# Kernel optimization log

Measured on AMD Instinct MI355X. Metric: run time of the kernel, lower is better.

Reference implementation:

```python
import jax, jax.numpy as jnp
import numpy as np

B, N, D = 4, 2048, 512
H, DA, DL = 8, 64, 64  # heads, attention_dim, linear_dim
EPS = 1e-6


def _layer_norm(x, eps=EPS):
    # F.layer_norm with no affine params
    mu = jnp.mean(x, axis=-1, keepdims=True)
    var = jnp.var(x, axis=-1, keepdims=True)
    return (x - mu) * jax.lax.rsqrt(var + eps)


def setup_inputs() -> dict:
    key = jax.random.key(0)
    k1, k2, k3, k4 = jax.random.split(key, 4)
    x = jax.random.normal(k1, (B, N, D), dtype=jnp.float32)
    # causal (lower-triangular) valid-attention mask, float {0,1}, shape (B,1,N,N)
    attention_mask = jnp.broadcast_to(
        jnp.tril(jnp.ones((N, N), dtype=jnp.float32))[None, None], (B, 1, N, N)
    )
    # _uvqk: (D, 2*H*DL + 2*H*DA), init normal(0, 0.02)
    uvqk = 0.02 * jax.random.normal(k2, (D, 2 * H * DL + 2 * H * DA), dtype=jnp.float32)
    # _o: Linear(H*DL -> D), xavier uniform
    fan_in, fan_out = H * DL, D
    limit = float(np.sqrt(6.0 / (fan_in + fan_out)))
    o_weight = jax.random.uniform(k3, (fan_out, fan_in), dtype=jnp.float32, minval=-limit, maxval=limit)
    o_bias = jnp.zeros((D,), dtype=jnp.float32)
    return {"x": x, "attention_mask": attention_mask, "uvqk": uvqk,
            "o_weight": o_weight, "o_bias": o_bias}


def reference(x, attention_mask, uvqk, o_weight, o_bias):
    b, n, _ = x.shape
    normed_x = _layer_norm(x)
    mm = jax.nn.silu(normed_x @ uvqk)  # fused uvqk projection + silu
    u, v, q, k = jnp.split(mm, [H * DL, 2 * H * DL, 2 * H * DL + H * DA], axis=-1)
    qh = q.reshape(b, n, H, DA)
    kh = k.reshape(b, n, H, DA)
    vh = v.reshape(b, n, H, DL)
    # silu-activated (non-softmax) attention with mask
    qk = jnp.einsum('bnhd,bmhd->bhnm', qh, kh)
    qk = jax.nn.silu(qk) / n
    qk = qk * attention_mask  # (B,1,N,N) broadcast over heads
    attn = jnp.einsum('bhnm,bmhd->bnhd', qk, vh).reshape(b, n, H * DL)
    # gated norm + output proj + residual
    o_input = u * _layer_norm(attn)
    return o_input @ o_weight.T + o_bias + x
```

## Files before the change

### kernel.cpp

```cpp
#include <hip/hip_runtime.h>

typedef __bf16 bf16x8 __attribute__((ext_vector_type(8)));
typedef float f32x4 __attribute__((ext_vector_type(4)));
typedef float f32x16 __attribute__((ext_vector_type(16)));

__device__ __forceinline__ unsigned short f2bf(float f) {
  return __builtin_bit_cast(unsigned short, (__bf16)f);
}
__device__ __forceinline__ float bfu2f(unsigned short b) {
  unsigned int u = ((unsigned int)b) << 16;
  return __builtin_bit_cast(float, u);
}
__device__ __forceinline__ float silu_f(float x) {
  return x * __builtin_amdgcn_rcpf(1.0f + __expf(-x));
}
__device__ __forceinline__ unsigned pk2(float a, float b) {
  return (unsigned)f2bf(a) | ((unsigned)f2bf(b) << 16);
}

template<int CPR, int NI, int SWZ>
__device__ __forceinline__ void stage16(const __bf16* __restrict__ g, int ld,
                                        __bf16* lds, int wave, int lane) {
#pragma unroll
  for (int t = 0; t < NI; ++t) {
    int cb = (wave * NI + t) * 64;
    int c = cb + lane;
    int row = c / CPR;
    int colb = (c % CPR) ^ (row & SWZ);
    __builtin_amdgcn_global_load_lds(
        (const __attribute__((address_space(1))) unsigned int*)(g + row * ld + colb * 8),
        (__attribute__((address_space(3))) unsigned int*)(lds + cb * 8),
        16, 0, 0);
  }
}

__global__ void k_prep(const float* __restrict__ x, __bf16* __restrict__ nx,
                       const float* __restrict__ ow, __bf16* __restrict__ owb,
                       const float* __restrict__ uvqk, __bf16* __restrict__ uvqkT) {
  int bid = blockIdx.x, tid = threadIdx.x;
  if (bid < 4096) {
    int t = tid & 127;
    int r = bid * 2 + (tid >> 7);
    int wave = tid >> 6;
    float4 v = ((const float4*)(x + (size_t)r * 512))[t];
    float s = v.x + v.y + v.z + v.w;
    float ss = v.x * v.x + v.y * v.y + v.z * v.z + v.w * v.w;
#pragma unroll
    for (int o = 32; o > 0; o >>= 1) { s += __shfl_down(s, o); ss += __shfl_down(ss, o); }
    __shared__ float red[4][2];
    if ((tid & 63) == 0) { red[wave][0] = s; red[wave][1] = ss; }
    __syncthreads();
    int rw = (wave >> 1) * 2;
    s = red[rw][0] + red[rw + 1][0];
    ss = red[rw][1] + red[rw + 1][1];
    float mu = s * (1.0f / 512.0f);
    float var = ss * (1.0f / 512.0f) - mu * mu;
    float rs = rsqrtf(var + 1e-6f);
    ushort4 o4;
    o4.x = f2bf((v.x - mu) * rs); o4.y = f2bf((v.y - mu) * rs);
    o4.z = f2bf((v.z - mu) * rs); o4.w = f2bf((v.w - mu) * rs);
    ((ushort4*)(nx + (size_t)r * 512))[t] = o4;
  } else if (bid < 4352) {
    int i = (bid - 4096) * 256 + tid;
    float4 v = ((const float4*)ow)[i];
    ushort4 o4;
    o4.x = f2bf(v.x); o4.y = f2bf(v.y); o4.z = f2bf(v.z); o4.w = f2bf(v.w);
    ((ushort4*)owb)[i] = o4;
  } else {
    __shared__ float tile[32][33];
    int bb = bid - 4352;
    int n0 = (bb & 63) * 32, k0 = (bb >> 6) * 32;
    int tx = tid & 31, ty = tid >> 5;
    for (int i = ty; i < 32; i += 8)
      tile[i][tx] = uvqk[(k0 + i) * 2048 + n0 + tx];
    __syncthreads();
    for (int i = ty; i < 32; i += 8)
      uvqkT[(n0 + i) * 512 + k0 + tx] = (__bf16)tile[tx][i];
  }
}

__global__ __launch_bounds__(256, 2) void k_proj(
    const __bf16* __restrict__ A, const __bf16* __restrict__ Bt,
    __bf16* __restrict__ u, __bf16* __restrict__ qn,
    __bf16* __restrict__ kn, __bf16* __restrict__ vt) {
  __shared__ __bf16 As[128 * 64];
  __shared__ __bf16 Bs[256 * 64];
  int tid = threadIdx.x, wave = tid >> 6, lane = tid & 63;
  int lr = lane & 15, lq = lane >> 4;
  int bn = blockIdx.x, bm = blockIdx.y;
  const __bf16* Ag = A + (size_t)bm * 128 * 512;
  const __bf16* Bg = Bt + (size_t)bn * 256 * 512;
  int wm = (wave >> 1) * 64, wn2 = (wave & 1) * 128;
  f32x4 acc[4][8] = {};
  for (int k0 = 0; k0 < 512; k0 += 64) {
    stage16<8, 4, 7>(Ag + k0, 512, As, wave, lane);
    stage16<8, 8, 7>(Bg + k0, 512, Bs, wave, lane);
    __syncthreads();
#pragma unroll
    for (int kk = 0; kk < 2; ++kk) {
      int b = kk * 4 + lq;
      bf16x8 a[4], bb[8];
#pragma unroll
      for (int i = 0; i < 4; ++i) {
        int row = wm + i * 16 + lr;
        a[i] = *(const bf16x8*)(As + row * 64 + ((b ^ (row & 7)) * 8));
      }
#pragma unroll
      for (int j = 0; j < 8; ++j) {
        int row = wn2 + j * 16 + lr;
        bb[j] = *(const bf16x8*)(Bs + row * 64 + ((b ^ (row & 7)) * 8));
      }
#pragma unroll
      for (int i = 0; i < 4; ++i)
#pragma unroll
        for (int j = 0; j < 8; ++j)
          acc[i][j] = __builtin_amdgcn_mfma_f32_16x16x32_bf16(a[i], bb[j], acc[i][j], 0, 0, 0);
    }
    __syncthreads();
  }
  int seg = bn >> 1;
  int cb = (bn & 1) * 256 + wn2;
  int rb0 = bm * 128 + wm + lq * 4;
  if (seg == 1) {
#pragma unroll
    for (int i = 0; i < 4; ++i) {
      int rb = rb0 + i * 16;
      int b = rb >> 11, n = rb & 2047;
#pragma unroll
      for (int j = 0; j < 8; ++j) {
        int c = cb + j * 16 + lr;
        ushort4 w;
        w.x = f2bf(silu_f(acc[i][j][0]) * (1.0f / 2048.0f));
        w.y = f2bf(silu_f(acc[i][j][1]) * (1.0f / 2048.0f));
        w.z = f2bf(silu_f(acc[i][j][2]) * (1.0f / 2048.0f));
        w.w = f2bf(silu_f(acc[i][j][3]) * (1.0f / 2048.0f));
        *(ushort4*)(vt + ((size_t)(b * 512 + c)) * 2048 + n) = w;
      }
    }
  } else {
    __bf16* dst = (seg == 0) ? u : ((seg == 2) ? qn : kn);
#pragma unroll
    for (int i = 0; i < 4; ++i) {
      int rb = rb0 + i * 16;
#pragma unroll
      for (int j = 0; j < 8; ++j) {
        int c = cb + j * 16 + lr;
#pragma unroll
        for (int rg = 0; rg < 4; ++rg)
          dst[(size_t)(rb + rg) * 512 + c] = (__bf16)silu_f(acc[i][j][rg]);
      }
    }
  }
}

__global__ __launch_bounds__(256, 4) void k_attn(
    const __bf16* __restrict__ qn, const __bf16* __restrict__ kn,
    const __bf16* __restrict__ vt, __bf16* __restrict__ oa,
    __bf16* __restrict__ ob, __bf16* __restrict__ oc) {
  __shared__ __bf16 lds[16384];
  __bf16* Kb0 = lds;
  __bf16* Kb1 = lds + 4096;
  __bf16* Vb0 = lds + 8192;
  __bf16* Vb1 = lds + 12288;
  __bf16* bo = lds;

  int bh = blockIdx.x, p = blockIdx.y, z = blockIdx.z;
  int b = bh >> 3, hd = bh & 7;
  int tid = threadIdx.x, wave = tid >> 6, lane = tid & 63;
  int l31 = lane & 31, lh = lane >> 5;
  const __bf16* Kg = kn + (size_t)(b * 2048) * 512 + hd * 64;
  const __bf16* Vg = vt + (size_t)(b * 512 + hd * 64) * 2048;
  __bf16* Oz = (z == 0) ? oa : ((z == 1) ? ob : oc);

  for (int ph = 0; ph < 2; ++ph) {
    int t = ph ? (15 - p) : p;
    int T = 2 * t + 2;
    int mlo = z * T / 3;
    int cnt = (z + 1) * T / 3 - mlo;
    int n0 = t * 128 + wave * 32;
    if (ph) __syncthreads();
    const __bf16* Qg = qn + (size_t)(b * 2048 + n0 + l31) * 512 + hd * 64 + lh * 8;
    bf16x8 qf[4];
#pragma unroll
    for (int ks = 0; ks < 4; ++ks) qf[ks] = *(const bf16x8*)(Qg + ks * 16);
    if (cnt > 0) {
      stage16<8, 2, 7>(Kg + (size_t)mlo * 64 * 512, 512, Kb0, wave, lane);
      stage16<8, 2, 7>(Vg + mlo * 64, 2048, Vb0, wave, lane);
    }
    __syncthreads();

    f32x16 po[2] = {};

    for (int i = 0; i < cnt; ++i) {
      int mt = mlo + i;
      const __bf16* Kc = (i & 1) ? Kb1 : Kb0;
      const __bf16* Vc = (i & 1) ? Vb1 : Vb0;
      if (i + 1 < cnt) {
        __bf16* Kn_ = (i & 1) ? Kb0 : Kb1;
        __bf16* Vn_ = (i & 1) ? Vb0 : Vb1;
        stage16<8, 2, 7>(Kg + (size_t)(mt + 1) * 64 * 512, 512, Kn_, wave, lane);
        stage16<8, 2, 7>(Vg + (mt + 1) * 64, 2048, Vn_, wave, lane);
      }
#pragma unroll
      for (int ms = 0; ms < 2; ++ms) {
        int m0 = mt * 64 + ms * 32;
        if (m0 > n0 + 31) continue;
        f32x16 s = {};
#pragma unroll
        for (int ks = 0; ks < 4; ++ks) {
          int row = ms * 32 + l31;
          bf16x8 ak = *(const bf16x8*)(Kc + row * 64 + (((ks * 2 + lh) ^ (row & 7)) * 8));
          s = __builtin_amdgcn_mfma_f32_32x32x16_bf16(ak, qf[ks], s, 0, 0, 0);
        }
        bool dtile = (m0 + 31 > n0);
        float vv[16];
#pragma unroll
        for (int r = 0; r < 16; ++r) {
          float xx = s[r];
          float pv = xx * __builtin_amdgcn_rcpf(1.0f + __expf(-xx));
          if (dtile) {
            int mrow = m0 + 4 * lh + (r & 3) + 8 * (r >> 2);
            int ncol = n0 + l31;
            if (mrow > ncol) pv = 0.0f;
          }
          vv[r] = pv;
        }
        unsigned pk[8];
#pragma unroll
        for (int q = 0; q < 8; ++q) pk[q] = pk2(vv[2 * q], vv[2 * q + 1]);
        bool lo_ = (lh == 0);
        unsigned xa = __shfl_xor(lo_ ? pk[2] : pk[0], 32);
        unsigned xb = __shfl_xor(lo_ ? pk[3] : pk[1], 32);
        unsigned xc = __shfl_xor(lo_ ? pk[6] : pk[4], 32);
        unsigned xd = __shfl_xor(lo_ ? pk[7] : pk[5], 32);
        union { bf16x8 v; unsigned u[4]; } f0, f1;
        f0.u[0] = lo_ ? pk[0] : xa;  f0.u[1] = lo_ ? pk[1] : xb;
        f0.u[2] = lo_ ? xa : pk[2];  f0.u[3] = lo_ ? xb : pk[3];
        f1.u[0] = lo_ ? pk[4] : xc;  f1.u[1] = lo_ ? pk[5] : xd;
        f1.u[2] = lo_ ? xc : pk[6];  f1.u[3] = lo_ ? xd : pk[7];
        bf16x8 pf[2] = { f0.v, f1.v };
#pragma unroll
        for (int t2 = 0; t2 < 2; ++t2) {
#pragma unroll
          for (int idl = 0; idl < 2; ++idl) {
            int row = idl * 32 + l31;
            bf16x8 av = *(const bf16x8*)(Vc + row * 64 +
                (((ms * 4 + t2 * 2 + lh) ^ (row & 7)) * 8));
            po[idl] = __builtin_amdgcn_mfma_f32_32x32x16_bf16(av, pf[t2], po[idl], 0, 0, 0);
          }
        }
      }
      __syncthreads();
    }

    {
      int nrow = wave * 32 + l31;
#pragma unroll
      for (int idl = 0; idl < 2; ++idl) {
#pragma unroll
        for (int g = 0; g < 4; ++g) {
          int dl0 = idl * 32 + g * 8 + lh * 4;
          int addr = nrow * 64 + ((((dl0 >> 3) ^ (nrow & 7)) << 3) | (dl0 & 7));
          ushort4 w;
          w.x = f2bf(po[idl][4 * g + 0]); w.y = f2bf(po[idl][4 * g + 1]);
          w.z = f2bf(po[idl][4 * g + 2]); w.w = f2bf(po[idl][4 * g + 3]);
          *(ushort4*)(bo + addr) = w;
        }
      }
    }
    __syncthreads();
    {
      int n = tid >> 1, cc = (tid & 1) * 32;
      __bf16* gdst = Oz + (size_t)(b * 2048 + t * 128 + n) * 512 + hd * 64 + cc;
#pragma unroll
      for (int kk2 = 0; kk2 < 4; ++kk2) {
        int dlb = cc + kk2 * 8;
        int a = n * 64 + (((dlb >> 3) ^ (n & 7)) << 3);
        *(uint4*)(gdst + kk2 * 8) = *(const uint4*)(bo + a);
      }
    }
  }
}

__global__ void k_oinput(const __bf16* __restrict__ oa, const __bf16* __restrict__ ob,
                         const __bf16* __restrict__ oc, const __bf16* __restrict__ u,
                         __bf16* __restrict__ oin) {
  int r = blockIdx.x, t = threadIdx.x;
  ushort4 a4 = ((const ushort4*)(oa + (size_t)r * 512))[t];
  ushort4 b4 = ((const ushort4*)(ob + (size_t)r * 512))[t];
  ushort4 c4 = ((const ushort4*)(oc + (size_t)r * 512))[t];
  float a0 = bfu2f(a4.x) + bfu2f(b4.x) + bfu2f(c4.x);
  float a1 = bfu2f(a4.y) + bfu2f(b4.y) + bfu2f(c4.y);
  float a2 = bfu2f(a4.z) + bfu2f(b4.z) + bfu2f(c4.z);
  float a3 = bfu2f(a4.w) + bfu2f(b4.w) + bfu2f(c4.w);
  float s = a0 + a1 + a2 + a3;
  float ss = a0 * a0 + a1 * a1 + a2 * a2 + a3 * a3;
#pragma unroll
  for (int o = 32; o > 0; o >>= 1) { s += __shfl_down(s, o); ss += __shfl_down(ss, o); }
  __shared__ float red[4];
  if ((t & 63) == 0) { red[(t >> 6) * 2] = s; red[(t >> 6) * 2 + 1] = ss; }
  __syncthreads();
  s = red[0] + red[2]; ss = red[1] + red[3];
  float mu = s * (1.0f / 512.0f);
  float var = ss * (1.0f / 512.0f) - mu * mu;
  float rs = rsqrtf(var + 1e-6f);
  ushort4 u4 = ((const ushort4*)(u + (size_t)r * 512))[t];
  ushort4 o4;
  o4.x = f2bf(bfu2f(u4.x) * (a0 - mu) * rs);
  o4.y = f2bf(bfu2f(u4.y) * (a1 - mu) * rs);
  o4.z = f2bf(bfu2f(u4.z) * (a2 - mu) * rs);
  o4.w = f2bf(bfu2f(u4.w) * (a3 - mu) * rs);
  ((ushort4*)(oin + (size_t)r * 512))[t] = o4;
}

__global__ __launch_bounds__(256, 4) void k_out(
    const __bf16* __restrict__ A, const __bf16* __restrict__ Bt,
    const float* __restrict__ bias, const float* __restrict__ x,
    float* __restrict__ out) {
  __shared__ __bf16 As[64 * 64];
  __shared__ __bf16 Bs[128 * 64];
  int tid = threadIdx.x, wave = tid >> 6, lane = tid & 63;
  int lr = lane & 15, lq = lane >> 4;
  int bn = blockIdx.x, bm = blockIdx.y;
  const __bf16* Ag = A + (size_t)bm * 64 * 512;
  const __bf16* Bg = Bt + (size_t)bn * 128 * 512;
  int wm = (wave >> 1) * 32, wn = (wave & 1) * 64;
  f32x4 acc[2][4] = {};
  for (int k0 = 0; k0 < 512; k0 += 64) {
    stage16<8, 2, 7>(Ag + k0, 512, As, wave, lane);
    stage16<8, 4, 7>(Bg + k0, 512, Bs, wave, lane);
    __syncthreads();
#pragma unroll
    for (int kk = 0; kk < 2; ++kk) {
      int b = kk * 4 + lq;
      bf16x8 a[2], bb[4];
#pragma unroll
      for (int i = 0; i < 2; ++i) {
        int row = wm + i * 16 + lr;
        a[i] = *(const bf16x8*)(As + row * 64 + ((b ^ (row & 7)) * 8));
      }
#pragma unroll
      for (int j = 0; j < 4; ++j) {
        int row = wn + j * 16 + lr;
        bb[j] = *(const bf16x8*)(Bs + row * 64 + ((b ^ (row & 7)) * 8));
      }
#pragma unroll
      for (int i = 0; i < 2; ++i)
#pragma unroll
        for (int j = 0; j < 4; ++j)
          acc[i][j] = __builtin_amdgcn_mfma_f32_16x16x32_bf16(a[i], bb[j], acc[i][j], 0, 0, 0);
    }
    __syncthreads();
  }
  int cb = bn * 128 + wn;
  int rb0 = bm * 64 + wm + lq * 4;
#pragma unroll
  for (int j = 0; j < 4; ++j) {
    int c = cb + j * 16 + lr;
    float bv = bias[c];
#pragma unroll
    for (int i = 0; i < 2; ++i) {
      int rb = rb0 + i * 16;
#pragma unroll
      for (int rg = 0; rg < 4; ++rg) {
        size_t idx = (size_t)(rb + rg) * 512 + c;
        out[idx] = acc[i][j][rg] + bv + x[idx];
      }
    }
  }
}

extern "C" void kernel_launch(void* const* d_in, const int* in_sizes, int n_in,
                              void* d_out, int out_size, void* d_ws, size_t ws_size,
                              hipStream_t stream) {
  const float* x = (const float*)d_in[0];
  const float* uvqk = (const float*)d_in[2];
  const float* ow = (const float*)d_in[3];
  const float* obias = (const float*)d_in[4];
  float* out = (float*)d_out;

  char* w = (char*)d_ws;
  const size_t MB8 = 8u * 1024 * 1024;
  __bf16* nx    = (__bf16*)(w);
  __bf16* u     = (__bf16*)(w + MB8);
  __bf16* qn    = (__bf16*)(w + 2 * MB8);
  __bf16* kn    = (__bf16*)(w + 3 * MB8);
  __bf16* vt    = (__bf16*)(w + 4 * MB8);
  __bf16* uvqkT = (__bf16*)(w + 5 * MB8);
  __bf16* owb   = (__bf16*)(w + 5 * MB8 + 2097152);
  __bf16* Oa    = nx;
  __bf16* Ob    = (__bf16*)d_out;
  __bf16* Oc    = (__bf16*)d_out + (size_t)8192 * 512;
  __bf16* o_in  = qn;

  k_prep<<<5376, 256, 0, stream>>>(x, nx, ow, owb, uvqk, uvqkT);
  k_proj<<<dim3(8, 64), 256, 0, stream>>>(nx, uvqkT, u, qn, kn, vt);
  k_attn<<<dim3(32, 8, 3), 256, 0, stream>>>(qn, kn, vt, Oa, Ob, Oc);
  k_oinput<<<8192, 128, 0, stream>>>(Oa, Ob, Oc, u, o_in);
  k_out<<<dim3(4, 128), 256, 0, stream>>>(o_in, owb, obias, x, out);
}
```

Baseline: 198.9 us.

## Split attention KV range four ways, swap shuffles for permlane32, interleave QK MFMAs

The attention kernel can now split each query tile's key range into four partial sums instead of three when the workspace is large enough, giving more blocks. An extra partial buffer is added, and the reduce kernel reads and sums it. Separately, the cross-half lane exchange uses permlane32_swap instead of shfl_xor, with a runtime probe to work out the swap ordering. Both QK^T MFMA chains of a 64-key tile are now issued before either silu/PV stage. Waves are also rotated over query sub-tiles per block to balance the causal work. Risks: more partial-buffer traffic, an extra read in the reduce kernel, and higher register pressure.

```diff
diff --git a/kernel.cpp b/kernel.cpp
--- a/kernel.cpp
+++ b/kernel.cpp
@@ -3,6 +3,7 @@
 typedef __bf16 bf16x8 __attribute__((ext_vector_type(8)));
 typedef float f32x4 __attribute__((ext_vector_type(4)));
 typedef float f32x16 __attribute__((ext_vector_type(16)));
+typedef int i32x2 __attribute__((ext_vector_type(2)));
 
 __device__ __forceinline__ unsigned short f2bf(float f) {
   return __builtin_bit_cast(unsigned short, (__bf16)f);
@@ -153,10 +154,57 @@
   }
 }
 
+__device__ __forceinline__ void attn_finish(
+    const f32x16& s, int m0, int n0, int l31, int lh, int ms, bool natural,
+    const __bf16* Vc, f32x16 po[2]) {
+  bool dt = (m0 + 31 > n0);
+  unsigned pk[8];
+#pragma unroll
+  for (int q = 0; q < 8; ++q) {
+    float p01[2];
+#pragma unroll
+    for (int h = 0; h < 2; ++h) {
+      int r = 2 * q + h;
+      float xx = s[r];
+      float pv = xx * __builtin_amdgcn_rcpf(1.0f + __expf(-xx));
+      if (dt) {
+        int mrow = m0 + 4 * lh + (r & 3) + 8 * (r >> 2);
+        if (mrow > n0 + l31) pv = 0.0f;
+      }
+      p01[h] = pv;
+    }
+    pk[q] = pk2(p01[0], p01[1]);
+  }
+  i32x2 r0 = __builtin_amdgcn_permlane32_swap((int)pk[0], (int)pk[2], false, false);
+  i32x2 r1 = __builtin_amdgcn_permlane32_swap((int)pk[1], (int)pk[3], false, false);
+  i32x2 r2 = __builtin_amdgcn_permlane32_swap((int)pk[4], (int)pk[6], false, false);
+  i32x2 r3 = __builtin_amdgcn_permlane32_swap((int)pk[5], (int)pk[7], false, false);
+  union { bf16x8 v; unsigned u[4]; } f0, f1;
+  if (natural) {
+    f0.u[0] = r0.x; f0.u[2] = r0.y; f0.u[1] = r1.x; f0.u[3] = r1.y;
+    f1.u[0] = r2.x; f1.u[2] = r2.y; f1.u[1] = r3.x; f1.u[3] = r3.y;
+  } else {
+    f0.u[0] = r0.y; f0.u[2] = r0.x; f0.u[1] = r1.y; f0.u[3] = r1.x;
+    f1.u[0] = r2.y; f1.u[2] = r2.x; f1.u[1] = r3.y; f1.u[3] = r3.x;
+  }
+  bf16x8 pf[2] = { f0.v, f1.v };
+#pragma unroll
+  for (int t2 = 0; t2 < 2; ++t2) {
+#pragma unroll
+    for (int idl = 0; idl < 2; ++idl) {
+      int row = idl * 32 + l31;
+      bf16x8 av = *(const bf16x8*)(Vc + row * 64 +
+          (((ms * 4 + t2 * 2 + lh) ^ (row & 7)) * 8));
+      po[idl] = __builtin_amdgcn_mfma_f32_32x32x16_bf16(av, pf[t2], po[idl], 0, 0, 0);
+    }
+  }
+}
+
 __global__ __launch_bounds__(256, 4) void k_attn(
     const __bf16* __restrict__ qn, const __bf16* __restrict__ kn,
     const __bf16* __restrict__ vt, __bf16* __restrict__ oa,
-    __bf16* __restrict__ ob, __bf16* __restrict__ oc) {
+    __bf16* __restrict__ ob, __bf16* __restrict__ oc,
+    __bf16* __restrict__ od, int nz) {
   __shared__ __bf16 lds[16384];
   __bf16* Kb0 = lds;
   __bf16* Kb1 = lds + 4096;
@@ -168,16 +216,20 @@
   int b = bh >> 3, hd = bh & 7;
   int tid = threadIdx.x, wave = tid >> 6, lane = tid & 63;
   int l31 = lane & 31, lh = lane >> 5;
+  int wsl = (wave + p + z + bh) & 3;
   const __bf16* Kg = kn + (size_t)(b * 2048) * 512 + hd * 64;
   const __bf16* Vg = vt + (size_t)(b * 512 + hd * 64) * 2048;
-  __bf16* Oz = (z == 0) ? oa : ((z == 1) ? ob : oc);
+  __bf16* Oz = (z == 0) ? oa : ((z == 1) ? ob : ((z == 2) ? oc : od));
+
+  i32x2 pr = __builtin_amdgcn_permlane32_swap(lh ? 10 : 11, lh ? 20 : 21, false, false);
+  bool natural = (__builtin_amdgcn_readfirstlane(pr.x) == 11);
 
   for (int ph = 0; ph < 2; ++ph) {
     int t = ph ? (15 - p) : p;
     int T = 2 * t + 2;
-    int mlo = z * T / 3;
-    int cnt = (z + 1) * T / 3 - mlo;
-    int n0 = t * 128 + wave * 32;
+    int mlo = z * T / nz;
+    int cnt = (z + 1) * T / nz - mlo;
+    int n0 = t * 128 + wsl * 32;
     if (ph) __syncthreads();
     const __bf16* Qg = qn + (size_t)(b * 2048 + n0 + l31) * 512 + hd * 64 + lh * 8;
     bf16x8 qf[4];
@@ -201,60 +253,33 @@
         stage16<8, 2, 7>(Kg + (size_t)(mt + 1) * 64 * 512, 512, Kn_, wave, lane);
         stage16<8, 2, 7>(Vg + (mt + 1) * 64, 2048, Vn_, wave, lane);
       }
-#pragma unroll
-      for (int ms = 0; ms < 2; ++ms) {
-        int m0 = mt * 64 + ms * 32;
-        if (m0 > n0 + 31) continue;
-        f32x16 s = {};
+      int m0a = mt * 64, m0b = mt * 64 + 32;
+      bool a0 = (m0a <= n0 + 31);
+      bool a1 = (m0b <= n0 + 31);
+      f32x16 s0 = {}, s1 = {};
+      if (a0) {
 #pragma unroll
         for (int ks = 0; ks < 4; ++ks) {
-          int row = ms * 32 + l31;
+          int row = l31;
           bf16x8 ak = *(const bf16x8*)(Kc + row * 64 + (((ks * 2 + lh) ^ (row & 7)) * 8));
-          s = __builtin_amdgcn_mfma_f32_32x32x16_bf16(ak, qf[ks], s, 0, 0, 0);
+          s0 = __builtin_amdgcn_mfma_f32_32x32x16_bf16(ak, qf[ks], s0, 0, 0, 0);
         }
-        bool dtile = (m0 + 31 > n0);
-        float vv[16];
-#pragma unroll
-        for (int r = 0; r < 16; ++r) {
-          float xx = s[r];
-          float pv = xx * __builtin_amdgcn_rcpf(1.0f + __expf(-xx));
-          if (dtile) {
-            int mrow = m0 + 4 * lh + (r & 3) + 8 * (r >> 2);
-            int ncol = n0 + l31;
-            if (mrow > ncol) pv = 0.0f;
-          }
-          vv[r] = pv;
+      }
+      if (a1) {
+#pragma unroll
+        for (int ks = 0; ks < 4; ++ks) {
+          int row = 32 + l31;
+          bf16x8 ak = *(const bf16x8*)(Kc + row * 64 + (((ks * 2 + lh) ^ (row & 7)) * 8));
+          s1 = __builtin_amdgcn_mfma_f32_32x32x16_bf16(ak, qf[ks], s1, 0, 0, 0);
         }
-        unsigned pk[8];
-#pragma unroll
-        for (int q = 0; q < 8; ++q) pk[q] = pk2(vv[2 * q], vv[2 * q + 1]);
-        bool lo_ = (lh == 0);
-        unsigned xa = __shfl_xor(lo_ ? pk[2] : pk[0], 32);
-        unsigned xb = __shfl_xor(lo_ ? pk[3] : pk[1], 32);
-        unsigned xc = __shfl_xor(lo_ ? pk[6] : pk[4], 32);
-        unsigned xd = __shfl_xor(lo_ ? pk[7] : pk[5], 32);
-        union { bf16x8 v; unsigned u[4]; } f0, f1;
-        f0.u[0] = lo_ ? pk[0] : xa;  f0.u[1] = lo_ ? pk[1] : xb;
-        f0.u[2] = lo_ ? xa : pk[2];  f0.u[3] = lo_ ? xb : pk[3];
-        f1.u[0] = lo_ ? pk[4] : xc;  f1.u[1] = lo_ ? pk[5] : xd;
-        f1.u[2] = lo_ ? xc : pk[6];  f1.u[3] = lo_ ? xd : pk[7];
-        bf16x8 pf[2] = { f0.v, f1.v };
-#pragma unroll
-        for (int t2 = 0; t2 < 2; ++t2) {
-#pragma unroll
-          for (int idl = 0; idl < 2; ++idl) {
-            int row = idl * 32 + l31;
-            bf16x8 av = *(const bf16x8*)(Vc + row * 64 +
-                (((ms * 4 + t2 * 2 + lh) ^ (row & 7)) * 8));
-            po[idl] = __builtin_amdgcn_mfma_f32_32x32x16_bf16(av, pf[t2], po[idl], 0, 0, 0);
-          }
-        }
-      }
+      }
+      if (a0) attn_finish(s0, m0a, n0, l31, lh, 0, natural, Vc, po);
+      if (a1) attn_finish(s1, m0b, n0, l31, lh, 1, natural, Vc, po);
       __syncthreads();
     }
 
     {
-      int nrow = wave * 32 + l31;
+      int nrow = wsl * 32 + l31;
 #pragma unroll
       for (int idl = 0; idl < 2; ++idl) {
 #pragma unroll
@@ -283,16 +308,22 @@
 }
 
 __global__ void k_oinput(const __bf16* __restrict__ oa, const __bf16* __restrict__ ob,
-                         const __bf16* __restrict__ oc, const __bf16* __restrict__ u,
-                         __bf16* __restrict__ oin) {
+                         const __bf16* __restrict__ oc, const __bf16* __restrict__ od,
+                         const __bf16* __restrict__ u, __bf16* __restrict__ oin,
+                         int nz) {
   int r = blockIdx.x, t = threadIdx.x;
   ushort4 a4 = ((const ushort4*)(oa + (size_t)r * 512))[t];
   ushort4 b4 = ((const ushort4*)(ob + (size_t)r * 512))[t];
   ushort4 c4 = ((const ushort4*)(oc + (size_t)r * 512))[t];
-  float a0 = bfu2f(a4.x) + bfu2f(b4.x) + bfu2f(c4.x);
-  float a1 = bfu2f(a4.y) + bfu2f(b4.y) + bfu2f(c4.y);
-  float a2 = bfu2f(a4.z) + bfu2f(b4.z) + bfu2f(c4.z);
-  float a3 = bfu2f(a4.w) + bfu2f(b4.w) + bfu2f(c4.w);
+  float e0 = 0.f, e1 = 0.f, e2 = 0.f, e3 = 0.f;
+  if (nz == 4) {
+    ushort4 d4 = ((const ushort4*)(od + (size_t)r * 512))[t];
+    e0 = bfu2f(d4.x); e1 = bfu2f(d4.y); e2 = bfu2f(d4.z); e3 = bfu2f(d4.w);
+  }
+  float a0 = bfu2f(a4.x) + bfu2f(b4.x) + bfu2f(c4.x) + e0;
+  float a1 = bfu2f(a4.y) + bfu2f(b4.y) + bfu2f(c4.y) + e1;
+  float a2 = bfu2f(a4.z) + bfu2f(b4.z) + bfu2f(c4.z) + e2;
+  float a3 = bfu2f(a4.w) + bfu2f(b4.w) + bfu2f(c4.w) + e3;
   float s = a0 + a1 + a2 + a3;
   float ss = a0 * a0 + a1 * a1 + a2 * a2 + a3 * a3;
 #pragma unroll
@@ -388,14 +419,18 @@
   __bf16* vt    = (__bf16*)(w + 4 * MB8);
   __bf16* uvqkT = (__bf16*)(w + 5 * MB8);
   __bf16* owb   = (__bf16*)(w + 5 * MB8 + 2097152);
+  size_t od_off = 5 * MB8 + 2097152 + 524288;
   __bf16* Oa    = nx;
   __bf16* Ob    = (__bf16*)d_out;
   __bf16* Oc    = (__bf16*)d_out + (size_t)8192 * 512;
+  __bf16* Od    = (__bf16*)(w + od_off);
   __bf16* o_in  = qn;
+
+  int nz = (ws_size >= od_off + MB8) ? 4 : 3;
 
   k_prep<<<5376, 256, 0, stream>>>(x, nx, ow, owb, uvqk, uvqkT);
   k_proj<<<dim3(8, 64), 256, 0, stream>>>(nx, uvqkT, u, qn, kn, vt);
-  k_attn<<<dim3(32, 8, 3), 256, 0, stream>>>(qn, kn, vt, Oa, Ob, Oc);
-  k_oinput<<<8192, 128, 0, stream>>>(Oa, Ob, Oc, u, o_in);
+  k_attn<<<dim3(32, 8, nz), 256, 0, stream>>>(qn, kn, vt, Oa, Ob, Oc, Od, nz);
+  k_oinput<<<8192, 128, 0, stream>>>(Oa, Ob, Oc, Od, u, o_in, nz);
   k_out<<<dim3(4, 128), 256, 0, stream>>>(o_in, owb, obias, x, out);
 }
```

Result: no change. 200.5 us (+0.8%).
